# Kernel tuning notes

Hardware: AMD Instinct MI355X
Metric: run time of the kernel (lower is better)

Reference implementation:

```python
import jax, jax.numpy as jnp
import numpy as np

B, L, H, E = 4, 2048, 8, 64

def setup_inputs() -> dict:
    key = jax.random.key(0)
    kq, kk, kv = jax.random.split(key, 3)
    queries = jax.random.normal(kq, (B, L, H, E), dtype=jnp.float32)
    keys = jax.random.normal(kk, (B, L, H, E), dtype=jnp.float32)
    values = jax.random.normal(kv, (B, L, H, E), dtype=jnp.float32)
    return {"queries": queries, "keys": keys, "values": values}

def reference(queries, keys, values):
    # queries/keys/values: [B, L, H, E]
    E_ = queries.shape[-1]
    scale = 1.0 / jnp.sqrt(jnp.float32(E_))
    # scores: [B, H, L, S]
    scores = jnp.einsum('blhe,bshe->bhls', queries, keys)
    Lq, S = scores.shape[-2], scores.shape[-1]
    # TriangularCausalMask: mask positions where s > l (strict upper triangle)
    causal = jnp.tril(jnp.ones((Lq, S), dtype=bool))
    scores = jnp.where(causal, scores, -jnp.inf)
    A = jax.nn.softmax(scale * scores, axis=-1)  # dropout p=0 -> identity
    V = jnp.einsum('bhls,bshd->blhd', A, values)
    return V
```

## Files before the change

### kernel.cpp

```cpp
#include <hip/hip_runtime.h>
#include <hip/hip_bf16.h>


#define Bc 4
#define Lc 2048
#define Hc 8
#define Ec 64
#define TB 64
#define NT (Lc / TB)
#define BH_BYTES (NT * TB * Ec * 2)
#define WS_V_OFF ((size_t)32 * BH_BYTES)

using f32x4 = __attribute__((ext_vector_type(4))) float;
using f16x8 = __attribute__((ext_vector_type(8))) _Float16;
using f16x4 = __attribute__((ext_vector_type(4))) _Float16;
using hf16x2 = __fp16 __attribute__((ext_vector_type(2)));

static __device__ __forceinline__ unsigned int pk2(float lo, float hi) {
    union { hf16x2 h; unsigned int u; } c;
    c.h = __builtin_amdgcn_cvt_pkrtz(lo, hi);
    return c.u;
}

static __device__ __forceinline__ void gload16(const void* g, void* l) {
    __builtin_amdgcn_global_load_lds(
        (const __attribute__((address_space(1))) unsigned int*)g,
        (__attribute__((address_space(3))) unsigned int*)l, 16, 0, 0);
}

__global__ __launch_bounds__(256)
void prep_kernel(const float* __restrict__ K, const float* __restrict__ V,
                 char* __restrict__ ws)
{
    __shared__ char vstage[64 * 144];

    const int bid = blockIdx.x;
    const int bh = bid >> 5, kt = bid & 31;
    const int b = bh >> 3, h = bh & 7;
    const int tid = threadIdx.x;
    const int r = tid >> 2, q4 = tid & 3;
    const int c0 = 16 * q4;
    const size_t base_bh = (size_t)b * Lc * Hc * Ec + (size_t)h * Ec;
    const int kbase = kt * TB;
    char* kimg = ws + (size_t)bh * BH_BYTES + (size_t)kt * 8192;
    char* vimg = ws + WS_V_OFF + (size_t)bh * BH_BYTES + (size_t)kt * 8192;

    const int rs = (r & 7) << 4;
    {
        const float* kp = K + base_bh + (size_t)(kbase + r) * 512 + c0;
        unsigned int w[8];
        #pragma unroll
        for (int i = 0; i < 4; ++i) {
            float4 f = *(const float4*)(kp + 4 * i);
            w[2*i]   = pk2(f.x, f.y);
            w[2*i+1] = pk2(f.z, f.w);
        }
        *(uint4*)(kimg + r * 128 + ((32*q4)      ^ rs)) = *(uint4*)&w[0];
        *(uint4*)(kimg + r * 128 + ((32*q4 + 16) ^ rs)) = *(uint4*)&w[4];
    }
    {
        const float* vp = V + base_bh + (size_t)(kbase + r) * 512 + c0;
        unsigned int w[8];
        #pragma unroll
        for (int i = 0; i < 4; ++i) {
            float4 f = *(const float4*)(vp + 4 * i);
            w[2*i]   = pk2(f.x, f.y);
            w[2*i+1] = pk2(f.z, f.w);
        }
        *(uint4*)(vstage + r * 144 + 32*q4)      = *(uint4*)&w[0];
        *(uint4*)(vstage + r * 144 + 32*q4 + 16) = *(uint4*)&w[4];
    }
    __syncthreads();
    {
        const int e = tid >> 2, kq = tid & 3, kv0 = 16 * kq;
        unsigned int w[8];
        #pragma unroll
        for (int i = 0; i < 8; ++i) {
            unsigned int lo = *(const unsigned short*)(vstage + (kv0 + 2*i)     * 144 + 2*e);
            unsigned int hi = *(const unsigned short*)(vstage + (kv0 + 2*i + 1) * 144 + 2*e);
            w[i] = lo | (hi << 16);
        }
        const int es = (e & 7) << 4;
        *(uint4*)(vimg + e * 128 + ((32*kq)      ^ es)) = *(uint4*)&w[0];
        *(uint4*)(vimg + e * 128 + ((32*kq + 16) ^ es)) = *(uint4*)&w[4];
    }
}

__global__ __launch_bounds__(256)
void fa_fwd_kernel(const float* __restrict__ Q, const char* __restrict__ ws,
                   float* __restrict__ Out)
{
    __shared__ char klds[2 * 8192];
    __shared__ char vlds[2 * 8192];

    const int bid = blockIdx.x;
    const int qi  = bid >> 5;
    const int bh  = bid & 31;
    const int b   = bh >> 3, h = bh & 7;
    const int qt  = (NT - 1) - qi;
    const int qbase = qt * TB;

    const int tid  = threadIdx.x;
    const int wid  = tid >> 6;
    const int lane = tid & 63;
    const int l15  = lane & 15;
    const int l4   = lane >> 4;

    const size_t base_bh = (size_t)b * Lc * Hc * Ec + (size_t)h * Ec;
    const char* kimg = ws + (size_t)bh * BH_BYTES;
    const char* vimg = ws + WS_V_OFF + (size_t)bh * BH_BYTES;

    const int qrow0 = qbase + 16 * wid;
    f16x8 qa[2];
    {
        const float* qpr = Q + base_bh + (size_t)(qrow0 + l15) * 512;
        #pragma unroll
        for (int kc = 0; kc < 2; ++kc) {
            const float* p = qpr + 32 * kc + 8 * l4;
            float4 f0 = *(const float4*)(p);
            float4 f1 = *(const float4*)(p + 4);
            union { f16x8 v; unsigned int u[4]; } pk;
            pk.u[0] = pk2(f0.x, f0.y);
            pk.u[1] = pk2(f0.z, f0.w);
            pk.u[2] = pk2(f1.x, f1.y);
            pk.u[3] = pk2(f1.z, f1.w);
            qa[kc] = pk.v;
        }
    }

    f32x4 o[4] = {};
    float m_run = -1e30f, l_run = 0.f;
    const float SL2E = 0.125f * 1.44269504088896340736f;

    const int stoff = wid * 2048 + lane * 16;
    gload16(kimg + stoff,        klds + stoff);
    gload16(kimg + stoff + 1024, klds + stoff + 1024);
    gload16(vimg + stoff,        vlds + stoff);
    gload16(vimg + stoff + 1024, vlds + stoff + 1024);
    __syncthreads();

    for (int kt = 0; kt <= qt; ++kt) {
        const int cur = kt & 1;
        const char* kb = klds + cur * 8192;
        const char* vb = vlds + cur * 8192;

        if (kt < qt) {
            const char* ks = kimg + (size_t)(kt + 1) * 8192;
            const char* vs = vimg + (size_t)(kt + 1) * 8192;
            char* kd = klds + (cur ^ 1) * 8192;
            char* vd = vlds + (cur ^ 1) * 8192;
            gload16(ks + stoff,        kd + stoff);
            gload16(ks + stoff + 1024, kd + stoff + 1024);
            gload16(vs + stoff,        vd + stoff);
            gload16(vs + stoff + 1024, vd + stoff + 1024);
        }

        f32x4 s[4];
        #pragma unroll
        for (int n = 0; n < 4; ++n) {
            const int row = 16 * n + l15;
            const int rsw = (row & 7) << 4;
            f16x8 a0 = *(const f16x8*)(kb + row * 128 + ((16 * l4)      ^ rsw));
            f16x8 a1 = *(const f16x8*)(kb + row * 128 + ((64 + 16 * l4) ^ rsw));
            f32x4 z = {0.f, 0.f, 0.f, 0.f};
            z = __builtin_amdgcn_mfma_f32_16x16x32_f16(a0, qa[0], z, 0, 0, 0);
            z = __builtin_amdgcn_mfma_f32_16x16x32_f16(a1, qa[1], z, 0, 0, 0);
            s[n] = z;
        }

        if (kt == qt) {
            const int q_g = qrow0 + l15;
            #pragma unroll
            for (int n = 0; n < 4; ++n) {
                #pragma unroll
                for (int r = 0; r < 4; ++r) {
                    const int kv_g = kt * TB + 16 * n + 4 * l4 + r;
                    if (kv_g > q_g) s[n][r] = -1e30f;
                }
            }
        }

        float pmax = -1e30f;
        #pragma unroll
        for (int n = 0; n < 4; ++n)
            #pragma unroll
            for (int r = 0; r < 4; ++r) pmax = fmaxf(pmax, s[n][r]);
        pmax = fmaxf(pmax, __shfl_xor(pmax, 16, 64));
        pmax = fmaxf(pmax, __shfl_xor(pmax, 32, 64));
        const float m_new = fmaxf(m_run, pmax);
        const float fac = __builtin_exp2f((m_run - m_new) * SL2E);
        m_run = m_new;

        float ps = 0.f;
        unsigned int ph[4][2];
        #pragma unroll
        for (int n = 0; n < 4; ++n) {
            float p0 = __builtin_exp2f((s[n][0] - m_new) * SL2E);
            float p1 = __builtin_exp2f((s[n][1] - m_new) * SL2E);
            float p2 = __builtin_exp2f((s[n][2] - m_new) * SL2E);
            float p3 = __builtin_exp2f((s[n][3] - m_new) * SL2E);
            ps += (p0 + p1) + (p2 + p3);
            ph[n][0] = pk2(p0, p1);
            ph[n][1] = pk2(p2, p3);
        }
        ps += __shfl_xor(ps, 16, 64);
        ps += __shfl_xor(ps, 32, 64);
        l_run = l_run * fac + ps;

        float fr[4];
        #pragma unroll
        for (int r = 0; r < 4; ++r) fr[r] = __shfl(fac, 20 * l4 + r, 64);
        #pragma unroll
        for (int c = 0; c < 4; ++c)
            #pragma unroll
            for (int r = 0; r < 4; ++r) o[c][r] *= fr[r];

        #pragma unroll
        for (int m = 0; m < 4; ++m) {
            union { f16x4 h; unsigned int u[2]; } pa;
            pa.u[0] = ph[m][0]; pa.u[1] = ph[m][1];
            #pragma unroll
            for (int c = 0; c < 4; ++c) {
                const int erow = 16 * c + l15;
                const f16x4 vbf = *(const f16x4*)(vb + erow * 128 +
                                   ((32 * m + 8 * l4) ^ ((erow & 7) << 4)));
                o[c] = __builtin_amdgcn_mfma_f32_16x16x16f16(pa.h, vbf, o[c], 0, 0, 0);
            }
        }
        __syncthreads();
    }

    const float inv = 1.f / l_run;
    float ir[4];
    #pragma unroll
    for (int r = 0; r < 4; ++r) ir[r] = __shfl(inv, 20 * l4 + r, 64);
    float* op = Out + base_bh;
    #pragma unroll
    for (int c = 0; c < 4; ++c)
        #pragma unroll
        for (int r = 0; r < 4; ++r)
            op[(size_t)(qrow0 + 4 * l4 + r) * 512 + 16 * c + l15] = o[c][r] * ir[r];
}

extern "C" void kernel_launch(void* const* d_in, const int* in_sizes, int n_in,
                              void* d_out, int out_size, void* d_ws, size_t ws_size,
                              hipStream_t stream) {
    const float* Q = (const float*)d_in[0];
    const float* K = (const float*)d_in[1];
    const float* V = (const float*)d_in[2];
    float* O = (float*)d_out;
    char* ws = (char*)d_ws;
    hipLaunchKernelGGL(prep_kernel, dim3(Bc * Hc * NT), dim3(256), 0, stream, K, V, ws);
    hipLaunchKernelGGL(fa_fwd_kernel, dim3(NT * Bc * Hc), dim3(256), 0, stream, Q, ws, O);
}
```

Baseline: 67.35 us.

## Pair causal query tiles per block, lazily rescale, fold scale into Q

Each block now handles two query tiles, a long one and its mirrored short one, so causal work is balanced across a grid half the size. The softmax scale is folded into Q at load time. The running max is only updated when it grows by more than a threshold, which skips most rescales. The row sum is built with an extra MFMA against a ones vector instead of shuffles. This trades per-block parallelism and precision headroom in fp16 probabilities for less ALU work and balanced tail load.

```diff
diff --git a/kernel.cpp b/kernel.cpp
--- a/kernel.cpp
+++ b/kernel.cpp
@@ -94,11 +94,9 @@
     __shared__ char vlds[2 * 8192];
 
     const int bid = blockIdx.x;
-    const int qi  = bid >> 5;
+    const int pi  = bid >> 5;
     const int bh  = bid & 31;
     const int b   = bh >> 3, h = bh & 7;
-    const int qt  = (NT - 1) - qi;
-    const int qbase = qt * TB;
 
     const int tid  = threadIdx.x;
     const int wid  = tid >> 6;
@@ -109,137 +107,159 @@
     const size_t base_bh = (size_t)b * Lc * Hc * Ec + (size_t)h * Ec;
     const char* kimg = ws + (size_t)bh * BH_BYTES;
     const char* vimg = ws + WS_V_OFF + (size_t)bh * BH_BYTES;
-
-    const int qrow0 = qbase + 16 * wid;
-    f16x8 qa[2];
-    {
-        const float* qpr = Q + base_bh + (size_t)(qrow0 + l15) * 512;
-        #pragma unroll
-        for (int kc = 0; kc < 2; ++kc) {
-            const float* p = qpr + 32 * kc + 8 * l4;
-            float4 f0 = *(const float4*)(p);
-            float4 f1 = *(const float4*)(p + 4);
+    const float SL2E = 0.125f * 1.44269504088896340736f;
+
+    const int sw  = (l15 & 7) << 4;
+    const int ko0 = l15 * 128 + ((16 * l4)      ^ sw);
+    const int ko1 = l15 * 128 + ((64 + 16 * l4) ^ sw);
+    int vo[4];
+    #pragma unroll
+    for (int m = 0; m < 4; ++m) vo[m] = l15 * 128 + ((32 * m + 8 * l4) ^ sw);
+
+    f16x4 ones;
+    {
+        const _Float16 ov = (_Float16)((l15 == 0) ? 1.0f : 0.0f);
+        ones[0] = ov; ones[1] = ov; ones[2] = ov; ones[3] = ov;
+    }
+
+    const int stoff = wid * 2048 + lane * 16;
+
+    #pragma unroll 1
+    for (int half = 0; half < 2; ++half) {
+        const int qt = half ? pi : (NT - 1 - pi);
+        const int qrow0 = qt * TB + 16 * wid;
+
+        f16x8 qa0, qa1;
+        {
+            const float* qpr = Q + base_bh + (size_t)(qrow0 + l15) * 512 + 8 * l4;
+            float4 f0 = *(const float4*)(qpr);
+            float4 f1 = *(const float4*)(qpr + 4);
+            float4 f2 = *(const float4*)(qpr + 32);
+            float4 f3 = *(const float4*)(qpr + 36);
             union { f16x8 v; unsigned int u[4]; } pk;
-            pk.u[0] = pk2(f0.x, f0.y);
-            pk.u[1] = pk2(f0.z, f0.w);
-            pk.u[2] = pk2(f1.x, f1.y);
-            pk.u[3] = pk2(f1.z, f1.w);
-            qa[kc] = pk.v;
-        }
-    }
-
-    f32x4 o[4] = {};
-    float m_run = -1e30f, l_run = 0.f;
-    const float SL2E = 0.125f * 1.44269504088896340736f;
-
-    const int stoff = wid * 2048 + lane * 16;
-    gload16(kimg + stoff,        klds + stoff);
-    gload16(kimg + stoff + 1024, klds + stoff + 1024);
-    gload16(vimg + stoff,        vlds + stoff);
-    gload16(vimg + stoff + 1024, vlds + stoff + 1024);
-    __syncthreads();
-
-    for (int kt = 0; kt <= qt; ++kt) {
-        const int cur = kt & 1;
-        const char* kb = klds + cur * 8192;
-        const char* vb = vlds + cur * 8192;
-
-        if (kt < qt) {
-            const char* ks = kimg + (size_t)(kt + 1) * 8192;
-            const char* vs = vimg + (size_t)(kt + 1) * 8192;
-            char* kd = klds + (cur ^ 1) * 8192;
-            char* vd = vlds + (cur ^ 1) * 8192;
-            gload16(ks + stoff,        kd + stoff);
-            gload16(ks + stoff + 1024, kd + stoff + 1024);
-            gload16(vs + stoff,        vd + stoff);
-            gload16(vs + stoff + 1024, vd + stoff + 1024);
-        }
-
-        f32x4 s[4];
-        #pragma unroll
-        for (int n = 0; n < 4; ++n) {
-            const int row = 16 * n + l15;
-            const int rsw = (row & 7) << 4;
-            f16x8 a0 = *(const f16x8*)(kb + row * 128 + ((16 * l4)      ^ rsw));
-            f16x8 a1 = *(const f16x8*)(kb + row * 128 + ((64 + 16 * l4) ^ rsw));
-            f32x4 z = {0.f, 0.f, 0.f, 0.f};
-            z = __builtin_amdgcn_mfma_f32_16x16x32_f16(a0, qa[0], z, 0, 0, 0);
-            z = __builtin_amdgcn_mfma_f32_16x16x32_f16(a1, qa[1], z, 0, 0, 0);
-            s[n] = z;
-        }
-
-        if (kt == qt) {
-            const int q_g = qrow0 + l15;
+            pk.u[0] = pk2(f0.x * SL2E, f0.y * SL2E);
+            pk.u[1] = pk2(f0.z * SL2E, f0.w * SL2E);
+            pk.u[2] = pk2(f1.x * SL2E, f1.y * SL2E);
+            pk.u[3] = pk2(f1.z * SL2E, f1.w * SL2E);
+            qa0 = pk.v;
+            pk.u[0] = pk2(f2.x * SL2E, f2.y * SL2E);
+            pk.u[1] = pk2(f2.z * SL2E, f2.w * SL2E);
+            pk.u[2] = pk2(f3.x * SL2E, f3.y * SL2E);
+            pk.u[3] = pk2(f3.z * SL2E, f3.w * SL2E);
+            qa1 = pk.v;
+        }
+
+        f32x4 o[4] = {};
+        f32x4 ol = {};
+        float m_run = -1e30f;
+
+        gload16(kimg + stoff,        klds + stoff);
+        gload16(kimg + stoff + 1024, klds + stoff + 1024);
+        gload16(vimg + stoff,        vlds + stoff);
+        gload16(vimg + stoff + 1024, vlds + stoff + 1024);
+        __syncthreads();
+
+        for (int kt = 0; kt <= qt; ++kt) {
+            const int cur = kt & 1;
+            const char* kb = klds + cur * 8192;
+            const char* vb = vlds + cur * 8192;
+
+            if (kt < qt) {
+                const char* ks = kimg + (size_t)(kt + 1) * 8192;
+                const char* vs = vimg + (size_t)(kt + 1) * 8192;
+                char* kd = klds + (cur ^ 1) * 8192;
+                char* vd = vlds + (cur ^ 1) * 8192;
+                gload16(ks + stoff,        kd + stoff);
+                gload16(ks + stoff + 1024, kd + stoff + 1024);
+                gload16(vs + stoff,        vd + stoff);
+                gload16(vs + stoff + 1024, vd + stoff + 1024);
+            }
+
+            f32x4 s[4];
             #pragma unroll
             for (int n = 0; n < 4; ++n) {
-                #pragma unroll
-                for (int r = 0; r < 4; ++r) {
-                    const int kv_g = kt * TB + 16 * n + 4 * l4 + r;
-                    if (kv_g > q_g) s[n][r] = -1e30f;
+                f16x8 a0 = *(const f16x8*)(kb + n * 2048 + ko0);
+                f16x8 a1 = *(const f16x8*)(kb + n * 2048 + ko1);
+                f32x4 z = {0.f, 0.f, 0.f, 0.f};
+                z = __builtin_amdgcn_mfma_f32_16x16x32_f16(a0, qa0, z, 0, 0, 0);
+                z = __builtin_amdgcn_mfma_f32_16x16x32_f16(a1, qa1, z, 0, 0, 0);
+                s[n] = z;
+            }
+
+            if (kt == qt) {
+                const int q_g = qrow0 + l15;
+                #pragma unroll
+                for (int n = 0; n < 4; ++n) {
+                    #pragma unroll
+                    for (int r = 0; r < 4; ++r) {
+                        const int kv_g = kt * TB + 16 * n + 4 * l4 + r;
+                        if (kv_g > q_g) s[n][r] = -1e30f;
+                    }
                 }
             }
-        }
-
-        float pmax = -1e30f;
-        #pragma unroll
-        for (int n = 0; n < 4; ++n)
-            #pragma unroll
-            for (int r = 0; r < 4; ++r) pmax = fmaxf(pmax, s[n][r]);
-        pmax = fmaxf(pmax, __shfl_xor(pmax, 16, 64));
-        pmax = fmaxf(pmax, __shfl_xor(pmax, 32, 64));
-        const float m_new = fmaxf(m_run, pmax);
-        const float fac = __builtin_exp2f((m_run - m_new) * SL2E);
-        m_run = m_new;
-
-        float ps = 0.f;
-        unsigned int ph[4][2];
-        #pragma unroll
-        for (int n = 0; n < 4; ++n) {
-            float p0 = __builtin_exp2f((s[n][0] - m_new) * SL2E);
-            float p1 = __builtin_exp2f((s[n][1] - m_new) * SL2E);
-            float p2 = __builtin_exp2f((s[n][2] - m_new) * SL2E);
-            float p3 = __builtin_exp2f((s[n][3] - m_new) * SL2E);
-            ps += (p0 + p1) + (p2 + p3);
-            ph[n][0] = pk2(p0, p1);
-            ph[n][1] = pk2(p2, p3);
-        }
-        ps += __shfl_xor(ps, 16, 64);
-        ps += __shfl_xor(ps, 32, 64);
-        l_run = l_run * fac + ps;
-
-        float fr[4];
-        #pragma unroll
-        for (int r = 0; r < 4; ++r) fr[r] = __shfl(fac, 20 * l4 + r, 64);
+
+            float a0 = fmaxf(s[0][0], s[0][1]), a1 = fmaxf(s[0][2], s[0][3]);
+            float a2 = fmaxf(s[1][0], s[1][1]), a3 = fmaxf(s[1][2], s[1][3]);
+            float a4 = fmaxf(s[2][0], s[2][1]), a5 = fmaxf(s[2][2], s[2][3]);
+            float a6 = fmaxf(s[3][0], s[3][1]), a7 = fmaxf(s[3][2], s[3][3]);
+            float pmax = fmaxf(fmaxf(fmaxf(a0, a1), fmaxf(a2, a3)),
+                               fmaxf(fmaxf(a4, a5), fmaxf(a6, a7)));
+            pmax = fmaxf(pmax, __shfl_xor(pmax, 16, 64));
+            pmax = fmaxf(pmax, __shfl_xor(pmax, 32, 64));
+
+            if (!__all(pmax - m_run <= 8.0f)) {
+                const float m_new = fmaxf(m_run, pmax);
+                const float fac = __builtin_exp2f(m_run - m_new);
+                m_run = m_new;
+                float fr[4];
+                #pragma unroll
+                for (int r = 0; r < 4; ++r) fr[r] = __shfl(fac, 4 * l4 + r, 64);
+                #pragma unroll
+                for (int c = 0; c < 4; ++c)
+                    #pragma unroll
+                    for (int r = 0; r < 4; ++r) o[c][r] *= fr[r];
+                #pragma unroll
+                for (int r = 0; r < 4; ++r) ol[r] *= fr[r];
+            }
+
+            unsigned int ph[4][2];
+            #pragma unroll
+            for (int n = 0; n < 4; ++n) {
+                float p0 = __builtin_exp2f(s[n][0] - m_run);
+                float p1 = __builtin_exp2f(s[n][1] - m_run);
+                float p2 = __builtin_exp2f(s[n][2] - m_run);
+                float p3 = __builtin_exp2f(s[n][3] - m_run);
+                ph[n][0] = pk2(p0, p1);
+                ph[n][1] = pk2(p2, p3);
+            }
+
+            #pragma unroll
+            for (int m = 0; m < 4; ++m) {
+                union { f16x4 h; unsigned int u[2]; } pa;
+                pa.u[0] = ph[m][0]; pa.u[1] = ph[m][1];
+                ol = __builtin_amdgcn_mfma_f32_16x16x16f16(pa.h, ones, ol, 0, 0, 0);
+                #pragma unroll
+                for (int c = 0; c < 4; ++c) {
+                    const f16x4 vbf = *(const f16x4*)(vb + c * 2048 + vo[m]);
+                    o[c] = __builtin_amdgcn_mfma_f32_16x16x16f16(pa.h, vbf, o[c], 0, 0, 0);
+                }
+            }
+            __syncthreads();
+        }
+
+        float ir[4];
+        #pragma unroll
+        for (int r = 0; r < 4; ++r) {
+            const float iv = 1.0f / ol[r];
+            ir[r] = __shfl(iv, 16 * l4, 64);
+        }
+        float* op = Out + base_bh;
         #pragma unroll
         for (int c = 0; c < 4; ++c)
             #pragma unroll
-            for (int r = 0; r < 4; ++r) o[c][r] *= fr[r];
-
-        #pragma unroll
-        for (int m = 0; m < 4; ++m) {
-            union { f16x4 h; unsigned int u[2]; } pa;
-            pa.u[0] = ph[m][0]; pa.u[1] = ph[m][1];
-            #pragma unroll
-            for (int c = 0; c < 4; ++c) {
-                const int erow = 16 * c + l15;
-                const f16x4 vbf = *(const f16x4*)(vb + erow * 128 +
-                                   ((32 * m + 8 * l4) ^ ((erow & 7) << 4)));
-                o[c] = __builtin_amdgcn_mfma_f32_16x16x16f16(pa.h, vbf, o[c], 0, 0, 0);
-            }
-        }
-        __syncthreads();
-    }
-
-    const float inv = 1.f / l_run;
-    float ir[4];
-    #pragma unroll
-    for (int r = 0; r < 4; ++r) ir[r] = __shfl(inv, 20 * l4 + r, 64);
-    float* op = Out + base_bh;
-    #pragma unroll
-    for (int c = 0; c < 4; ++c)
-        #pragma unroll
-        for (int r = 0; r < 4; ++r)
-            op[(size_t)(qrow0 + 4 * l4 + r) * 512 + 16 * c + l15] = o[c][r] * ir[r];
+            for (int r = 0; r < 4; ++r)
+                op[(size_t)(qrow0 + 4 * l4 + r) * 512 + 16 * c + l15] = o[c][r] * ir[r];
+    }
 }
 
 extern "C" void kernel_launch(void* const* d_in, const int* in_sizes, int n_in,
@@ -251,5 +271,5 @@
     float* O = (float*)d_out;
     char* ws = (char*)d_ws;
     hipLaunchKernelGGL(prep_kernel, dim3(Bc * Hc * NT), dim3(256), 0, stream, K, V, ws);
-    hipLaunchKernelGGL(fa_fwd_kernel, dim3(NT * Bc * Hc), dim3(256), 0, stream, Q, ws, O);
-}
+    hipLaunchKernelGGL(fa_fwd_kernel, dim3((NT / 2) * Bc * Hc), dim3(256), 0, stream, Q, ws, O);
+}
```

New measurement: 65.50 us. 2.7% less time.
